# Performance work log

Measured on AMD Instinct MI355X. Metric: run time of the kernel, lower is better.

## Reference

```python
import jax, jax.numpy as jnp
import numpy as np

NUM_NET = 5
N = 10000        # nodes per net
E = 160000       # edges per net
B = 512          # molecule graphs per batch
FXD = 62         # node feature dim
FXT = 954        # cell feature dim
D = 128          # output_dim
H1 = 10          # heads in first GATConv


def setup_inputs() -> dict:
    key = jax.random.key(0)
    ks = iter(jax.random.split(key, 64))
    f32 = jnp.float32
    p = lambda shape, scale=0.05: jax.random.normal(next(ks), shape, dtype=f32) * scale
    inp = {}
    inp['x1'] = jax.random.normal(next(ks), (NUM_NET, N, FXD), dtype=f32)
    inp['ei1'] = jax.random.randint(next(ks), (NUM_NET, 2, E), 0, N, dtype=jnp.int32)
    b = ((jnp.arange(N) * B) // N).astype(jnp.int32)  # sorted, no empty graphs
    inp['batch1'] = jnp.broadcast_to(b, (NUM_NET, N))
    inp['x2'] = jax.random.normal(next(ks), (NUM_NET, N, FXD), dtype=f32)
    inp['ei2'] = jax.random.randint(next(ks), (NUM_NET, 2, E), 0, N, dtype=jnp.int32)
    inp['batch2'] = jnp.broadcast_to(b, (NUM_NET, N))
    inp['cell'] = jax.random.normal(next(ks), (B, FXT), dtype=f32)
    # per-net GAT params (stacked over NUM_NET)
    inp['W1'] = p((NUM_NET, H1 * D, FXD))
    inp['a1s'] = p((NUM_NET, H1, D)); inp['a1d'] = p((NUM_NET, H1, D))
    inp['b1'] = p((NUM_NET, H1 * D))
    inp['W2'] = p((NUM_NET, D, H1 * D))
    inp['a2s'] = p((NUM_NET, 1, D)); inp['a2d'] = p((NUM_NET, 1, D))
    inp['b2'] = p((NUM_NET, D))
    inp['Wg'] = p((NUM_NET, D, D)); inp['bg'] = p((NUM_NET, D))
    # cell reduction MLP 954->2048->512->256
    inp['Wr1'] = p((2048, FXT)); inp['br1'] = p((2048,))
    inp['Wr2'] = p((512, 2048)); inp['br2'] = p((512,))
    inp['Wr3'] = p((2 * D, 512)); inp['br3'] = p((2 * D,))
    # head MLP 512->2048->512->128->2
    inp['Wf1'] = p((2048, 4 * D)); inp['bf1'] = p((2048,))
    inp['Wf2'] = p((512, 2048)); inp['bf2'] = p((512,))
    inp['Wf3'] = p((128, 512)); inp['bf3'] = p((128,))
    inp['Wo'] = p((2, 128)); inp['bo'] = p((2,))
    return inp


def _gat(x, src, dst, W, a_s, a_d, b):
    # PyG GATConv (eval): linear -> per-head attention logits -> segment softmax over dst -> scatter-sum
    n = x.shape[0]
    H, C = a_s.shape
    h = (x @ W.T).reshape(n, H, C)
    al = (h * a_s).sum(-1)   # [n, H] source term
    ar = (h * a_d).sum(-1)   # [n, H] dest term
    e = jax.nn.leaky_relu(al[src] + ar[dst], negative_slope=0.2)  # [Ee, H]
    m = jax.ops.segment_max(e, dst, num_segments=n)               # self-loops -> no empty segments
    pe = jnp.exp(e - m[dst])
    s = jax.ops.segment_sum(pe, dst, num_segments=n)
    alpha = pe / s[dst]
    out = jax.ops.segment_sum(h[src] * alpha[:, :, None], dst, num_segments=n)
    return out.reshape(n, H * C) + b


def _branch(x, ei, batch, W1, a1s, a1d, b1, W2, a2s, a2d, b2, Wg, bg):
    n = x.shape[0]
    loops = jnp.arange(n, dtype=ei.dtype)  # add_self_loops=True in PyG GATConv
    src = jnp.concatenate([ei[0], loops])
    dst = jnp.concatenate([ei[1], loops])
    h = jax.nn.elu(_gat(x, src, dst, W1, a1s, a1d, b1))
    h = jax.nn.elu(_gat(h, src, dst, W2, a2s, a2d, b2))
    g = jax.ops.segment_max(h, batch, num_segments=B)  # global max pool
    return jax.nn.relu(g @ Wg.T + bg)


def _l2n(v):
    return v / jnp.clip(jnp.linalg.norm(v, axis=1, keepdims=True), 1e-12)


def reference(x1, ei1, batch1, x2, ei2, batch2, cell,
              W1, a1s, a1d, b1, W2, a2s, a2d, b2, Wg, bg,
              Wr1, br1, Wr2, br2, Wr3, br3,
              Wf1, bf1, Wf2, bf2, Wf3, bf3, Wo, bo):
    x11 = jnp.zeros((B, D), dtype=x1.dtype)
    x22 = jnp.zeros((B, D), dtype=x2.dtype)
    for i in range(NUM_NET):
        pr = (W1[i], a1s[i], a1d[i], b1[i], W2[i], a2s[i], a2d[i], b2[i], Wg[i], bg[i])
        x11 = x11 + _branch(x1[i], ei1[i], batch1[i], *pr) / NUM_NET
        x22 = x22 + _branch(x2[i], ei2[i], batch2[i], *pr) / NUM_NET
    c = _l2n(cell)
    c = jax.nn.relu(c @ Wr1.T + br1)
    c = jax.nn.relu(c @ Wr2.T + br2)
    c = jax.nn.relu(c @ Wr3.T + br3)
    xc = _l2n(jnp.concatenate([x11, x22, c], axis=1))
    xc = jax.nn.relu(xc @ Wf1.T + bf1)
    xc = jax.nn.relu(xc @ Wf2.T + bf2)
    xc = jax.nn.relu(xc @ Wf3.T + bf3)
    return xc @ Wo.T + bo
```

## Files before the change

kernel.cpp:

```cpp
#include <hip/hip_runtime.h>
#include <hip/hip_bf16.h>
#include <math.h>

#define NUM_NET 5
#define NN 10000
#define NE 160000
#define BB 512
#define FXD 62
#define FXT 954
#define MP 10112

typedef __bf16 bf16x8 __attribute__((ext_vector_type(8)));
typedef float f32x4 __attribute__((ext_vector_type(4)));
typedef __hip_bfloat16 bf16;

__device__ __forceinline__ float ldf(const void* p, size_t i) {
  return ((const float*)p)[i];
}
__device__ __forceinline__ float lky(float v) { return v > 0.f ? v : 0.2f * v; }
__device__ __forceinline__ float eluf(float v) { return v > 0.f ? v : (__expf(v) - 1.f); }
__device__ __forceinline__ unsigned int packbf(float a, float b) {
  __hip_bfloat162 t;
  t.x = __float2bfloat16(a);
  t.y = __float2bfloat16(b);
// ... 82 lines not shown
  int br = z & 1, net = z >> 1;
  const int* base = (br ? ei2 : ei1) + (size_t)net * 2 * NE;
  const int* src = base;
  const int* dst = base + NE;
  const int* offz = offs + (size_t)z * (NN + 1);
  int* fillz = fill + (size_t)z * NN;
  int* out = csrc + (size_t)z * NE;
  int i = blockIdx.x * 256 + threadIdx.x;
  if (i < NE) {
    int d = dst[i];
    int p = offz[d] + atomicAdd(&fillz[d], 1);
    out[p] = src[i];
  }
}

__global__ __launch_bounds__(256) void walr_kernel(const void* __restrict__ W1,
                                                   const void* __restrict__ a1s,
                                                   const void* __restrict__ a1d,
                                                   bf16* __restrict__ walrb) {
  int net = blockIdx.x / 10, head = blockIdx.x % 10;
  int t = threadIdx.x, w = t >> 6, k = t & 63;
  __shared__ float ps[8][64];
  float accs = 0.f, accd = 0.f;
  for (int c = w; c < 128; c += 4) {
    float wv = (k < FXD)
        ? ldf(W1, (size_t)net * 1280 * FXD + (size_t)(head * 128 + c) * FXD + k) : 0.f;
    float vs = ldf(a1s, (size_t)net * 1280 + head * 128 + c);
    float vd = ldf(a1d, (size_t)net * 1280 + head * 128 + c);
    accs = fmaf(wv, vs, accs);
    accd = fmaf(wv, vd, accd);
  }
  ps[w][k] = accs;
  ps[4 + w][k] = accd;
  __syncthreads();
  if (w == 0) {
    float s = ps[0][k] + ps[1][k] + ps[2][k] + ps[3][k];
    float dd = ps[4][k] + ps[5][k] + ps[6][k] + ps[7][k];
    walrb[(size_t)net * 4096 + head * 64 + k] = __float2bfloat16(s);
    walrb[(size_t)net * 4096 + (16 + head) * 64 + k] = __float2bfloat16(dd);
  }
}

__global__ __launch_bounds__(256) void alpha_kernel(
    const float* __restrict__ alrA, const int* __restrict__ offsA,
    const int* __restrict__ srcsA, unsigned int* __restrict__ alphaG, int planeBase) {
  int z = blockIdx.z;
  int plane = planeBase + z;
  const float* alr = alrA + (size_t)plane * MP * 32;
  const int* offs = offsA + (size_t)plane * (NN + 1);
  const int* srcs = srcsA + (size_t)plane * NE;
  unsigned int* ag = alphaG + (size_t)z * (NE + NN) * 6;
  int wave = threadIdx.x >> 6, lane = threadIdx.x & 63;
  int d = blockIdx.x * 4 + wave;
  if (d >= NN) return;
  int e0 = offs[d], ne = offs[d + 1] - e0;
  int total = ne + 1;
  float arh[10];
#pragma unroll
  for (int h = 0; h < 10; h++) arh[h] = alr[(size_t)d * 32 + 16 + h];
  if (total <= 64) {
    int sc = (lane < ne) ? srcs[e0 + lane] : d;
    bool act = lane < total;
    const float* ap = &alr[(size_t)sc * 32];
    float v[10], m[10];
#pragma unroll
    for (int h = 0; h < 10; h++) {
      v[h] = act ? lky(ap[h] + arh[h]) : -1e30f;
      m[h] = v[h];
    }
#pragma unroll
    for (int o = 32; o > 0; o >>= 1)
#pragma unroll
      for (int h = 0; h < 10; h++) m[h] = fmaxf(m[h], __shfl_xor(m[h], o));
    float p[10], s[10];
#pragma unroll
    for (int h = 0; h < 10; h++) {
      p[h] = act ? __expf(v[h] - m[h]) : 0.f;
      s[h] = p[h];
    }
#pragma unroll
    for (int o = 32; o > 0; o >>= 1)
#pragma unroll
      for (int h = 0; h < 10; h++) s[h] += __shfl_xor(s[h], o);
    if (act) {
      float inv[10];
#pragma unroll
      for (int h = 0; h < 10; h++) inv[h] = 1.f / s[h];
      unsigned int wv[6];
#pragma unroll
      for (int hp = 0; hp < 5; hp++)
        wv[hp] = packbf(p[2 * hp] * inv[2 * hp], p[2 * hp + 1] * inv[2 * hp + 1]);
      wv[5] = (unsigned int)(d & 15);
      size_t row = (lane < ne) ? (size_t)(e0 + lane) : (size_t)(NE + d);
      unsigned int* rp = ag + row * 6;
#pragma unroll
      for (int j = 0; j < 6; j++) rp[j] = wv[j];
    }
  } else {
    float m[10], s[10];
#pragma unroll
    for (int h = 0; h < 10; h++) { m[h] = -1e30f; s[h] = 0.f; }
    for (int idx = lane; idx < total; idx += 64) {
      int sc = (idx < ne) ? srcs[e0 + idx] : d;
      const float* ap = &alr[(size_t)sc * 32];
#pragma unroll
      for (int h = 0; h < 10; h++) {
        float v = lky(ap[h] + arh[h]);
        if (v > m[h]) { s[h] = s[h] * __expf(m[h] - v) + 1.f; m[h] = v; }
        else s[h] += __expf(v - m[h]);
      }
    }
#pragma unroll
    for (int o = 32; o > 0; o >>= 1)
#pragma unroll
      for (int h = 0; h < 10; h++) {
        float mo = __shfl_xor(m[h], o), so = __shfl_xor(s[h], o);
        if (so > 0.f) {
          if (mo > m[h]) { s[h] = s[h] * __expf(m[h] - mo) + so; m[h] = mo; }
          else s[h] += so * __expf(mo - m[h]);
        }
      }
    for (int idx = lane; idx < total; idx += 64) {
      int sc = (idx < ne) ? srcs[e0 + idx] : d;
      const float* ap = &alr[(size_t)sc * 32];
      unsigned int wv[6];
#pragma unroll
      for (int hp = 0; hp < 5; hp++) {
        float v0 = lky(ap[2 * hp] + arh[2 * hp]);
        float v1 = lky(ap[2 * hp + 1] + arh[2 * hp + 1]);
        wv[hp] = packbf(__expf(v0 - m[2 * hp]) / s[2 * hp],
                        __expf(v1 - m[2 * hp + 1]) / s[2 * hp + 1]);
      }
      wv[5] = (unsigned int)(d & 15);
      size_t row = (idx < ne) ? (size_t)(e0 + idx) : (size_t)(NE + d);
      unsigned int* rp = ag + row * 6;
#pragma unroll
      for (int j = 0; j < 6; j++) rp[j] = wv[j];
    }
  }
}

struct Pref {
  uint4 xv;
  unsigned int a0, a1, a2, a3, a4;
  int dl;
  int av;
};

__device__ __forceinline__ void issue_pref(
    Pref& P, int kb, int e, int fblk, int tid, int nreal, int K_len, int e_begin,
    int d0, const int* __restrict__ srcs, const bf16* __restrict__ xp,
    const unsigned int* __restrict__ ag) {
  int ke = kb + e;
  int src;
  if (ke < nreal) {
    src = srcs[e_begin + ke];
  } else {
    int sl = ke - nreal;
    src = d0 + (sl < 16 ? sl : 0);
  }
  P.xv = *(const uint4*)&xp[(size_t)src * 64 + fblk * 8];
  P.av = 0;
  if (tid < 32 && ke < K_len) {
    P.av = 1;
    size_t row = (ke < nreal) ? (size_t)(e_begin + ke) : (size_t)(NE + d0 + (ke - nreal));
    const unsigned int* rp = ag + row * 6;
    P.a0 = rp[0]; P.a1 = rp[1]; P.a2 = rp[2]; P.a3 = rp[3]; P.a4 = rp[4];
    P.dl = (int)rp[5];
  }
}

__global__ __launch_bounds__(256) void xagg_kernel(
    const bf16* __restrict__ xpadA, const unsigned int* __restrict__ alphaG,
    const int* __restrict__ offsA, const int* __restrict__ srcsA,
    bf16* __restrict__ xagg2, int planeBase) {
  int z = blockIdx.z;
  int plane = planeBase + z;
  bf16* xagg = xagg2 + (size_t)z * 10 * MP * 64;
  int d0 = blockIdx.x * 16;
  int tid = threadIdx.x;

  if (d0 >= NN) {
    uint4 zz; zz.x = zz.y = zz.z = zz.w = 0u;
#pragma unroll
    for (int k = 0; k < 5; k++) {
      int i = tid + k * 256;
      int h = i >> 7, rem = i & 127, row = rem >> 3, seg = rem & 7;
      *(uint4*)&xagg[((size_t)h * MP + d0 + row) * 64 + seg * 8] = zz;
    }
    return;
  }

  const bf16* xp = xpadA + (size_t)plane * MP * 64;
  const int* offs = offsA + (size_t)plane * (NN + 1);
  const int* srcs = srcsA + (size_t)plane * NE;
  const unsigned int* ag = alphaG + (size_t)z * (NE + NN) * 6;

  __shared__ __align__(16) short A_s[10 * 16 * 40];
  __shared__ __align__(16) short Xt_s[64 * 40];

  int e_begin = offs[d0];
  int nreal = offs[d0 + 16] - e_begin;
  int K_len = nreal + 16;

  int e = tid & 31, fblk = tid >> 5;
  int lane = tid & 63, wave = tid >> 6;
  int l15 = lane & 15, quad = lane >> 4;
  int hbase = (wave >> 1) * 5;
  int wcol = (wave & 1) * 32;

  Pref Pn;
  issue_pref(Pn, 0, e, fblk, tid, nreal, K_len, e_begin, d0, srcs, xp, ag);

  {
    f32x4 z4 = (f32x4){0.f, 0.f, 0.f, 0.f};
    for (int i = tid; i < 800; i += 256) ((f32x4*)A_s)[i] = z4;
  }
  f32x4 acc[5][2];
#pragma unroll
  for (int i = 0; i < 5; i++)
#pragma unroll
    for (int j = 0; j < 2; j++) acc[i][j] = (f32x4){0.f, 0.f, 0.f, 0.f};
  int prev_dl = -1;
  __syncthreads();

  for (int kb = 0; kb < K_len; kb += 32) {
    Pref Pc = Pn;
    if (tid < 32) {
      if (prev_dl >= 0) {
#pragma unroll
        for (int h = 0; h < 10; h++) A_s[(h * 16 + prev_dl) * 40 + e] = 0;
      }
      prev_dl = -1;
      if (Pc.av) {
        int dlc = Pc.dl;
        A_s[(0 * 16 + dlc) * 40 + e] = (short)(Pc.a0 & 0xffff);
        A_s[(1 * 16 + dlc) * 40 + e] = (short)(Pc.a0 >> 16);
        A_s[(2 * 16 + dlc) * 40 + e] = (short)(Pc.a1 & 0xffff);
        A_s[(3 * 16 + dlc) * 40 + e] = (short)(Pc.a1 >> 16);
        A_s[(4 * 16 + dlc) * 40 + e] = (short)(Pc.a2 & 0xffff);
        A_s[(5 * 16 + dlc) * 40 + e] = (short)(Pc.a2 >> 16);
        A_s[(6 * 16 + dlc) * 40 + e] = (short)(Pc.a3 & 0xffff);
        A_s[(7 * 16 + dlc) * 40 + e] = (short)(Pc.a3 >> 16);
        A_s[(8 * 16 + dlc) * 40 + e] = (short)(Pc.a4 & 0xffff);
        A_s[(9 * 16 + dlc) * 40 + e] = (short)(Pc.a4 >> 16);
        prev_dl = dlc;
      }
    }
    {
      int fb8 = fblk * 8;
#pragma unroll
      for (int j = 0; j < 4; j++) {
        unsigned int w = ((const unsigned int*)&Pc.xv)[j];
        Xt_s[(fb8 + 2 * j) * 40 + e] = (short)(w & 0xffff);
        Xt_s[(fb8 + 2 * j + 1) * 40 + e] = (short)(w >> 16);
      }
    }
    if (kb + 32 < K_len)
      issue_pref(Pn, kb + 32, e, fblk, tid, nreal, K_len, e_begin, d0, srcs, xp, ag);
    __syncthreads();
    bf16x8 b0 = *(const bf16x8*)&Xt_s[(wcol + l15) * 40 + quad * 8];
    bf16x8 b1 = *(const bf16x8*)&Xt_s[(wcol + 16 + l15) * 40 + quad * 8];
#pragma unroll
    for (int hh = 0; hh < 5; hh++) {
      bf16x8 af = *(const bf16x8*)&A_s[((hbase + hh) * 16 + l15) * 40 + quad * 8];
      acc[hh][0] = __builtin_amdgcn_mfma_f32_16x16x32_bf16(af, b0, acc[hh][0], 0, 0, 0);
      acc[hh][1] = __builtin_amdgcn_mfma_f32_16x16x32_bf16(af, b1, acc[hh][1], 0, 0, 0);
    }
    __syncthreads();
  }

#pragma unroll
  for (int hh = 0; hh < 5; hh++) {
    int h = hbase + hh;
#pragma unroll
    for (int ft = 0; ft < 2; ft++) {
#pragma unroll
      for (int r = 0; r < 4; r++) {
        int drow = d0 + quad * 4 + r;
        xagg[((size_t)h * MP + drow) * 64 + wcol + ft * 16 + l15] =
            __float2bfloat16(acc[hh][ft][r]);
      }
    }
  }
}

__global__ __launch_bounds__(256) void fused_l1l2_kernel(
    const bf16* __restrict__ xagg2, const bf16* __restrict__ W1b,
    const void* __restrict__ b1raw, const bf16* __restrict__ W2b,
    const void* __restrict__ a2s, const void* __restrict__ a2d,
    float* __restrict__ al2A, float* __restrict__ ar2A,
    bf16* __restrict__ h2all, int planeBase) {
  int zz = blockIdx.z;
  int plane = planeBase + zz;
  int net = plane >> 1;
  long ow1 = (long)net * 1280 * 64;
  long ob1 = (long)net * 1280;
  long ow2 = (long)net * 128 * 1280;
  long oa2 = (long)net * 128;
  const bf16* xagg = xagg2 + (size_t)zz * 10 * MP * 64;
  float* al2p = al2A + (size_t)plane * NN;
  float* ar2p = ar2A + (size_t)plane * NN;
  bf16* h2 = h2all + (size_t)plane * MP * 128;
  int r0 = blockIdx.y * 64;
  __shared__ __align__(16) char uraw[35840];
  bf16* Ah = (bf16*)uraw;
  bf16* W1s = Ah + 64 * 72;
  bf16* Ps = (bf16*)uraw;
  bf16* W2s = Ps + 64 * 136;
  __shared__ float s_dot[2][2][32][2];
  int tid = threadIdx.x, lane = tid & 63, wave = tid >> 6;
  int l15 = lane & 15, quad = lane >> 4;
  int rowHalf = wave >> 1, colHalf = wave & 1;
  int wr = rowHalf * 32, wc = colHalf * 64;
  f32x4 acc2[2][4];
#pragma unroll
  for (int i = 0; i < 2; i++)
#pragma unroll
    for (int j = 0; j < 4; j++) acc2[i][j] = (f32x4){0.f, 0.f, 0.f, 0.f};

  for (int h = 0; h < 10; h++) {
    __syncthreads();
    for (int i = tid; i < 512; i += 256) {
      int r = i >> 3, seg = i & 7;
      *(uint4*)&Ah[r * 72 + seg * 8] =
          *(const uint4*)&xagg[((size_t)h * MP + r0 + r) * 64 + seg * 8];
    }
    for (int i = tid; i < 1024; i += 256) {
      int r = i >> 3, seg = i & 7;
      *(uint4*)&W1s[r * 72 + seg * 8] =
          *(const uint4*)&W1b[ow1 + (size_t)(h * 128 + r) * 64 + seg * 8];
    }
    __syncthreads();
    f32x4 acc1[4][2];
#pragma unroll
    for (int i = 0; i < 4; i++)
#pragma unroll
      for (int j = 0; j < 2; j++) acc1[i][j] = (f32x4){0.f, 0.f, 0.f, 0.f};
#pragma unroll
    for (int kc = 0; kc < 2; kc++) {
      bf16x8 af[4], bfr[2];
#pragma unroll
      for (int mi = 0; mi < 4; mi++)
        af[mi] = *(const bf16x8*)&Ah[(mi * 16 + l15) * 72 + kc * 32 + quad * 8];
#pragma unroll
      for (int ni = 0; ni < 2; ni++)
        bfr[ni] = *(const bf16x8*)&W1s[(wave * 32 + ni * 16 + l15) * 72 + kc * 32 + quad * 8];
#pragma unroll
      for (int mi = 0; mi < 4; mi++)
#pragma unroll
        for (int ni = 0; ni < 2; ni++)
          acc1[mi][ni] = __builtin_amdgcn_mfma_f32_16x16x32_bf16(af[mi], bfr[ni], acc1[mi][ni], 0, 0, 0);
    }
    __syncthreads();
#pragma unroll
    for (int ni = 0; ni < 2; ni++) {
      int pcol = wave * 32 + ni * 16 + l15;
      float bv = ldf(b1raw, ob1 + h * 128 + pcol);
#pragma unroll
      for (int mi = 0; mi < 4; mi++)
#pragma unroll
        for (int r = 0; r < 4; r++)
          Ps[(mi * 16 + quad * 4 + r) * 136 + pcol] =
              __float2bfloat16(eluf(acc1[mi][ni][r] + bv));
    }
    for (int i = tid; i < 1024; i += 256) {
      int r = i >> 3, seg = i & 7;
      *(uint4*)&W2s[r * 72 + seg * 8] =
          *(const uint4*)&W2b[ow2 + (size_t)r * 1280 + h * 128 + seg * 8];
    }
    __syncthreads();
#pragma unroll
    for (int kh = 0; kh < 2; kh++) {
      if (kh) {
        __syncthreads();
        for (int i = tid; i < 1024; i += 256) {
          int r = i >> 3, seg = i & 7;
          *(uint4*)&W2s[r * 72 + seg * 8] =
              *(const uint4*)&W2b[ow2 + (size_t)r * 1280 + h * 128 + 64 + seg * 8];
        }
        __syncthreads();
      }
#pragma unroll
      for (int kc = 0; kc < 2; kc++) {
        bf16x8 pa[2], pb[4];
#pragma unroll
        for (int mi = 0; mi < 2; mi++)
          pa[mi] = *(const bf16x8*)&Ps[(wr + mi * 16 + l15) * 136 + kh * 64 + kc * 32 + quad * 8];
#pragma unroll
        for (int ni = 0; ni < 4; ni++)
          pb[ni] = *(const bf16x8*)&W2s[(wc + ni * 16 + l15) * 72 + kc * 32 + quad * 8];
#pragma unroll
        for (int mi = 0; mi < 2; mi++)
#pragma unroll
          for (int ni = 0; ni < 4; ni++)
            acc2[mi][ni] = __builtin_amdgcn_mfma_f32_16x16x32_bf16(pa[mi], pb[ni], acc2[mi][ni], 0, 0, 0);
      }
    }
  }
  float asv[4], adv[4];
#pragma unroll
  for (int ni = 0; ni < 4; ni++) {
    int col = wc + ni * 16 + l15;
    asv[ni] = ldf(a2s, oa2 + col);
    adv[ni] = ldf(a2d, oa2 + col);
  }
#pragma unroll
  for (int mi = 0; mi < 2; mi++) {
#pragma unroll
    for (int r = 0; r < 4; r++) {
      int rl = mi * 16 + quad * 4 + r;
      int row = r0 + wr + rl;
      float psum = 0.f, pdum = 0.f;
#pragma unroll
      for (int ni = 0; ni < 4; ni++) {
        float v = acc2[mi][ni][r];
        h2[(size_t)row * 128 + wc + ni * 16 + l15] = __float2bfloat16(v);
        psum = fmaf(v, asv[ni], psum);
        pdum = fmaf(v, adv[ni], pdum);
      }
#pragma unroll
      for (int o = 1; o < 16; o <<= 1) {
        psum += __shfl_xor(psum, o);
        pdum += __shfl_xor(pdum, o);
      }
      if (l15 == 0) {
        s_dot[rowHalf][colHalf][rl][0] = psum;
        s_dot[rowHalf][colHalf][rl][1] = pdum;
      }
    }
  }
  __syncthreads();
  if (tid < 64) {
    int row = r0 + tid;
    if (row < NN) {
      int rh = tid >> 5, rl = tid & 31;
      al2p[row] = s_dot[rh][0][rl][0] + s_dot[rh][1][rl][0];
      ar2p[row] = s_dot[rh][0][rl][1] + s_dot[rh][1][rl][1];
    }
  }
}

__global__ __launch_bounds__(256) void mfma_gemm64(
    const bf16* __restrict__ A, long Az, const bf16* __restrict__ B, long Bz, int bdiv,
    const void* __restrict__ bias, long biasoff, long biaszs,
    float* __restrict__ Cf, long Cfz, int ldcf, int accum, int ncols, int brcol,
    bf16* __restrict__ Cb, long Cbz, int ldcb,
    int K, int act, float scale) {
  int z = blockIdx.z;
  int zb = bdiv ? (z >> 1) : z;
  A += (size_t)z * Az;
  B += (size_t)zb * Bz;
  if (Cf) Cf += (size_t)z * Cfz + (size_t)(z & 1) * brcol;
  if (Cb) Cb += (size_t)z * Cbz;
  const bf16* Ag = A + (size_t)blockIdx.y * 64 * K;
  const bf16* Bg = B + (size_t)blockIdx.x * 64 * K;
  __shared__ __align__(16) bf16 Asm[64 * 40];
  __shared__ __align__(16) bf16 Bsm[64 * 40];
  int tid = threadIdx.x;
  int lane = tid & 63, wave = tid >> 6;
  int wr = (wave >> 1) * 32, wc = (wave & 1) * 32;
  int l15 = lane & 15, quad = lane >> 4;
  f32x4 acc[2][2];
#pragma unroll
  for (int i = 0; i < 2; i++)
#pragma unroll
    for (int j = 0; j < 2; j++) acc[i][j] = (f32x4){0.f, 0.f, 0.f, 0.f};
  int isB = tid >> 7;
  int srow = (tid & 127) >> 1, shalf = tid & 1;
  const bf16* G = isB ? Bg : Ag;
  bf16* S = isB ? Bsm : Asm;
  for (int k0 = 0; k0 < K; k0 += 32) {
    const uint4* g = (const uint4*)(G + (size_t)srow * K + k0 + shalf * 16);
    uint4 v0 = g[0], v1 = g[1];
    __syncthreads();
    *(uint4*)&S[srow * 40 + shalf * 16] = v0;
    *(uint4*)&S[srow * 40 + shalf * 16 + 8] = v1;
    __syncthreads();
    bf16x8 af[2], bfr[2];
#pragma unroll
    for (int mi = 0; mi < 2; mi++)
      af[mi] = *(const bf16x8*)&Asm[(wr + mi * 16 + l15) * 40 + quad * 8];
#pragma unroll
    for (int ni = 0; ni < 2; ni++)
      bfr[ni] = *(const bf16x8*)&Bsm[(wc + ni * 16 + l15) * 40 + quad * 8];
#pragma unroll
    for (int mi = 0; mi < 2; mi++)
#pragma unroll
      for (int ni = 0; ni < 2; ni++)
        acc[mi][ni] = __builtin_amdgcn_mfma_f32_16x16x32_bf16(af[mi], bfr[ni], acc[mi][ni], 0, 0, 0);
  }
#pragma unroll
  for (int ni = 0; ni < 2; ni++) {
    int col = blockIdx.x * 64 + wc + ni * 16 + l15;
    if (col >= ncols) continue;
    float bv = bias ? ldf(bias, biasoff + (size_t)zb * biaszs + col) : 0.f;
#pragma unroll
    for (int mi = 0; mi < 2; mi++) {
      int rbase = blockIdx.y * 64 + wr + mi * 16 + quad * 4;
      f32x4 c = acc[mi][ni];
#pragma unroll
      for (int r = 0; r < 4; r++) {
        float v = c[r] + bv;
        if (act == 1) v = fmaxf(v, 0.f);
        else if (act == 2) v = eluf(v);
        v *= scale;
        if (Cf) {
          size_t ci = (size_t)(rbase + r) * ldcf + col;
          if (accum == 1) Cf[ci] += v;
          else if (accum == 2) atomicAdd(&Cf[ci], v);
          else Cf[ci] = v;
        }
        if (Cb) Cb[(size_t)(rbase + r) * ldcb + col] = __float2bfloat16(v);
      }
    }
  }
}

__global__ __launch_bounds__(256) void gat_agg1_kernel(
    const bf16* __restrict__ h2all, const float* __restrict__ alA, const float* __restrict__ arA,
    const int* __restrict__ offsA, const int* __restrict__ srcsA,
    const void* __restrict__ b2, bf16* __restrict__ out2all) {
  int z = blockIdx.z;
  int net = z >> 1;
  const bf16* h = h2all + (size_t)z * MP * 128;
  const float* al = alA + (size_t)z * NN;
  const float* ar = arA + (size_t)z * NN;
  const int* offs = offsA + (size_t)z * (NN + 1);
  const int* srcs = srcsA + (size_t)z * NE;
  __shared__ float2 s_pair[4][64];
  int wave = threadIdx.x >> 6, lane = threadIdx.x & 63;
  int d = blockIdx.x * 4 + wave;
  if (d >= NN) return;
  int e0 = offs[d], ne = offs[d + 1] - e0;
  int total = ne + 1;
  float ard = ar[d];
  float m, s, vcache = -1e30f;
  if (total <= 64) {
    int sc = (lane < ne) ? srcs[e0 + lane] : d;
    bool act = lane < total;
    vcache = act ? lky(al[sc] + ard) : -1e30f;
    m = vcache;
    s = act ? 1.f : 0.f;
#pragma unroll
    for (int o = 32; o > 0; o >>= 1) {
      float mo = __shfl_xor(m, o), so = __shfl_xor(s, o);
      if (so > 0.f) {
        if (mo > m) { s = s * __expf(m - mo) + so; m = mo; }
        else s += so * __expf(mo - m);
      }
    }
  } else {
    m = -1e30f; s = 0.f;
    for (int idx = lane; idx < total; idx += 64) {
      int sc = (idx < ne) ? srcs[e0 + idx] : d;
      float v = lky(al[sc] + ard);
      if (v > m) { s = s * __expf(m - v) + 1.f; m = v; }
      else s += __expf(v - m);
    }
#pragma unroll
    for (int o = 32; o > 0; o >>= 1) {
      float mo = __shfl_xor(m, o), so = __shfl_xor(s, o);
      if (so > 0.f) {
        if (mo > m) { s = s * __expf(m - mo) + so; m = mo; }
        else s += so * __expf(mo - m);
      }
    }
  }
  float inv_s = 1.f / s;
  float acc0 = 0.f, acc1v = 0.f;
  for (int c0 = 0; c0 < total; c0 += 64) {
    int idx = c0 + lane;
    int cnt = min(64, total - c0);
    if (idx < total) {
      int sc = (idx < ne) ? srcs[e0 + idx] : d;
      float v = (total <= 64) ? vcache : lky(al[sc] + ard);
      float a = __expf(v - m) * inv_s;
      s_pair[wave][lane] = make_float2(__int_as_float(sc), a);
    }
    int i = 0;
    for (; i + 2 <= cnt; i += 2) {
      float2 pA = s_pair[wave][i];
      float2 pB = s_pair[wave][i + 1];
      __hip_bfloat162 vA =
          ((const __hip_bfloat162*)(h + (size_t)__float_as_int(pA.x) * 128))[lane];
      __hip_bfloat162 vB =
          ((const __hip_bfloat162*)(h + (size_t)__float_as_int(pB.x) * 128))[lane];
      acc0 = fmaf(__bfloat162float(vA.x), pA.y, acc0);
      acc1v = fmaf(__bfloat162float(vA.y), pA.y, acc1v);
      acc0 = fmaf(__bfloat162float(vB.x), pB.y, acc0);
      acc1v = fmaf(__bfloat162float(vB.y), pB.y, acc1v);
    }
    if (i < cnt) {
      float2 pA = s_pair[wave][i];
      __hip_bfloat162 vA =
          ((const __hip_bfloat162*)(h + (size_t)__float_as_int(pA.x) * 128))[lane];
      acc0 = fmaf(__bfloat162float(vA.x), pA.y, acc0);
      acc1v = fmaf(__bfloat162float(vA.y), pA.y, acc1v);
    }
  }
  float b0 = ldf(b2, (size_t)net * 128 + 2 * lane);
  float b1v = ldf(b2, (size_t)net * 128 + 2 * lane + 1);
  __hip_bfloat162 o;
  o.x = __float2bfloat16(eluf(acc0 + b0));
  o.y = __float2bfloat16(eluf(acc1v + b1v));
  ((__hip_bfloat162*)(out2all + ((size_t)z * NN + d) * 128))[lane] = o;
}

__global__ __launch_bounds__(256) void pool_max_kernel(const bf16* __restrict__ out2all,
                                                       bf16* __restrict__ gall) {
  int z = blockIdx.z;
  const bf16* h = out2all + (size_t)z * NN * 128;
  bf16* g = gall + (size_t)z * BB * 128;
  int wave = threadIdx.x >> 6, lane = threadIdx.x & 63;
  int b = blockIdx.x * 4 + wave;
  if (b >= BB) return;
  int n0 = (b * NN + BB - 1) / BB;
  int n1 = ((b + 1) * NN + BB - 1) / BB;
  if (n1 > NN) n1 = NN;
  float mx = -1e30f, my = -1e30f;
  for (int n = n0; n < n1; n++) {
    __hip_bfloat162 v = ((const __hip_bfloat162*)(h + (size_t)n * 128))[lane];
    mx = fmaxf(mx, __bfloat162float(v.x));
    my = fmaxf(my, __bfloat162float(v.y));
  }
  __hip_bfloat162 o;
  o.x = __float2bfloat16(mx);
  o.y = __float2bfloat16(my);
  ((__hip_bfloat162*)(g + (size_t)b * 128))[lane] = o;
}

__global__ __launch_bounds__(256) void l2norm_b_kernel(const float* __restrict__ x,
                                                       bf16* __restrict__ y, int Din, int Kp) {
  int r = blockIdx.x, t = threadIdx.x;
  __shared__ float red[256];
  float s = 0.f;
  for (int i = t; i < Din; i += 256) {
    float v = x[(size_t)r * Din + i];
    s += v * v;
  }
  red[t] = s;
  __syncthreads();
  for (int o = 128; o > 0; o >>= 1) { if (t < o) red[t] += red[t + o]; __syncthreads(); }
  float inv = 1.f / fmaxf(sqrtf(red[0]), 1e-12f);
  for (int i = t; i < Kp; i += 256) {
    float v = (i < Din) ? x[(size_t)r * Din + i] : 0.f;
    y[(size_t)r * Kp + i] = __float2bfloat16(v * inv);
  }
}

__global__ void final_out_kernel(const float* __restrict__ f3, const void* __restrict__ Wo,
                                 const void* __restrict__ bo, float* __restrict__ out) {
  int r = blockIdx.x;
  int lane = threadIdx.x;
  float x0 = f3[(size_t)r * 128 + lane], x1v = f3[(size_t)r * 128 + 64 + lane];
  float s0 = x0 * ldf(Wo, lane) + x1v * ldf(Wo, 64 + lane);
  float s1 = x0 * ldf(Wo, 128 + lane) + x1v * ldf(Wo, 192 + lane);
#pragma unroll
  for (int o = 32; o > 0; o >>= 1) { s0 += __shfl_down(s0, o); s1 += __shfl_down(s1, o); }
  if (lane == 0) {
    out[r * 2] = s0 + ldf(bo, 0);
    out[r * 2 + 1] = s1 + ldf(bo, 1);
  }
}


extern "C" void kernel_launch(void* const* d_in, const int* in_sizes, int n_in,
                              void* d_out, int out_size, void* d_ws, size_t ws_size,
                              hipStream_t stream) {
  const void* x1 = d_in[0];
  const int* ei1 = (const int*)d_in[1];
  const void* x2 = d_in[3];
  const int* ei2 = (const int*)d_in[4];
  const void* cell = d_in[6];
  const void* W1 = d_in[7];
  const void* a1s = d_in[8];
  const void* a1d = d_in[9];
  const void* b1 = d_in[10];
  const void* W2 = d_in[11];
  const void* a2s = d_in[12];
  const void* a2d = d_in[13];
  const void* b2 = d_in[14];
  const void* Wg = d_in[15];
  const void* bg = d_in[16];
  const void* Wr1 = d_in[17]; const void* br1 = d_in[18];
  const void* Wr2 = d_in[19]; const void* br2 = d_in[20];
  const void* Wr3 = d_in[21]; const void* br3 = d_in[22];
  const void* Wf1 = d_in[23]; const void* bf1 = d_in[24];
  const void* Wf2 = d_in[25]; const void* bf2 = d_in[26];
  const void* Wf3 = d_in[27]; const void* bf3 = d_in[28];
  const void* Wo = d_in[29]; const void* bo = d_in[30];

  char* base = (char*)d_ws;
  size_t off = 0;
  auto alloc = [&](size_t bytes) -> void* {
    void* p = base + off;
    off = (off + bytes + 255) & ~(size_t)255;
    return p;
  };
  bf16* d_xpad = (bf16*)alloc((size_t)10 * MP * 64 * 2);
  bf16* d_W1b = (bf16*)alloc((size_t)5 * 1280 * 64 * 2);
  bf16* d_W2b = (bf16*)alloc((size_t)5 * 128 * 1280 * 2);
  bf16* d_Wgb = (bf16*)alloc((size_t)5 * 128 * 128 * 2);
  bf16* d_Wr1b = (bf16*)alloc((size_t)2048 * 960 * 2);
  bf16* d_Wr2b = (bf16*)alloc((size_t)512 * 2048 * 2);
  bf16* d_Wr3b = (bf16*)alloc((size_t)256 * 512 * 2);
  bf16* d_Wf1b = (bf16*)alloc((size_t)2048 * 512 * 2);
  bf16* d_Wf2b = (bf16*)alloc((size_t)512 * 2048 * 2);
  bf16* d_Wf3b = (bf16*)alloc((size_t)128 * 512 * 2);
  int* d_offs = (int*)alloc((size_t)10 * (NN + 1) * 4);
  int* d_srcs = (int*)alloc((size_t)10 * NE * 4);
  int* d_cnt = (int*)alloc((size_t)10 * NN * 4);
  bf16* d_walrb = (bf16*)alloc((size_t)5 * 64 * 64 * 2);
  float* d_alr = (float*)alloc((size_t)10 * MP * 32 * 4);
  float* d_al2 = (float*)alloc((size_t)20 * NN * 4);
  float* d_ar2 = d_al2 + (size_t)10 * NN;
  bf16* d_h2all = (bf16*)alloc((size_t)10 * MP * 128 * 2);
  unsigned int* d_alphaG = (unsigned int*)alloc((size_t)10 * (NE + NN) * 24);
  char* uni = base + off;
  size_t avail = (ws_size > off) ? (ws_size - off) : 0;
  size_t need10 = (size_t)10 * 10 * MP * 64 * 2;
  int G = (avail >= need10 + 65536) ? 10 : 5;
  bf16* d_xagg2 = (bf16*)uni;
  bf16* d_out2all = (bf16*)uni;
  bf16* d_gall = (bf16*)(uni + 25600000);
  float* d_xc = (float*)(uni + 26910720);
  bf16* d_xcb = (bf16*)(uni + 27959296);
  bf16* d_cnb = (bf16*)(uni + 28483584);
  bf16* d_m1b = (bf16*)(uni + 29466624);
  bf16* d_m2b = (bf16*)(uni + 31563776);
  float* d_f3 = (float*)(uni + 32088064);

  ConvTable tab;
  tab.d[0] = {x1, d_xpad, NN, FXD, MP, 64, 2, 0, 5, (MP + 3) / 4};
  tab.d[1] = {x2, d_xpad, NN, FXD, MP, 64, 2, 1, 5, (MP + 3) / 4};
  tab.d[2] = {W1, d_W1b, 1280, FXD, 1280, 64, 1, 0, 5, 320};
  tab.d[3] = {W2, d_W2b, 128, 1280, 128, 1280, 1, 0, 5, 32};
  tab.d[4] = {Wg, d_Wgb, 128, 128, 128, 128, 1, 0, 5, 32};
  tab.d[5] = {Wr1, d_Wr1b, 2048, FXT, 2048, 960, 1, 0, 1, 512};
  tab.d[6] = {Wr2, d_Wr2b, 512, 2048, 512, 2048, 1, 0, 1, 128};
  tab.d[7] = {Wr3, d_Wr3b, 256, 512, 256, 512, 1, 0, 1, 64};
  tab.d[8] = {Wf1, d_Wf1b, 2048, 512, 2048, 512, 1, 0, 1, 512};
  tab.d[9] = {Wf2, d_Wf2b, 512, 2048, 512, 2048, 1, 0, 1, 128};
  tab.d[10] = {Wf3, d_Wf3b, 128, 512, 128, 512, 1, 0, 1, 32};
  {
    int cum = 0;
    tab.blk0[0] = 0;
    for (int i = 0; i < 11; i++) {
      cum += tab.d[i].rowBlocks * tab.d[i].batch;
      tab.blk0[i + 1] = cum;
    }
    convert_all_kernel<<<dim3(cum), 256, 0, stream>>>(tab);
  }

  hipMemsetAsync(d_cnt, 0, (size_t)10 * NN * 4, stream);
  hist_kernel<<<dim3((NE + 255) / 256, 1, 10), 256, 0, stream>>>(ei1, ei2, d_cnt);
  scan_kernel<<<10, 256, 0, stream>>>(d_cnt, d_offs);
  hipMemsetAsync(d_cnt, 0, (size_t)10 * NN * 4, stream);
  scatter_kernel<<<dim3((NE + 255) / 256, 1, 10), 256, 0, stream>>>(ei1, ei2, d_offs, d_cnt, d_srcs);

  walr_kernel<<<50, 256, 0, stream>>>(W1, a1s, a1d, d_walrb);
  mfma_gemm64<<<dim3(1, MP / 64, 10), 256, 0, stream>>>(
      d_xpad, (long)MP * 64, d_walrb, 4096, 1, nullptr, 0, 0,
      d_alr, (long)MP * 32, 32, 0, 32, 0, nullptr, 0, 0, 64, 0, 1.f);

  for (int pb = 0; pb < 10; pb += G) {
    alpha_kernel<<<dim3(NN / 4, 1, G), 256, 0, stream>>>(d_alr, d_offs, d_srcs, d_alphaG, pb);
    xagg_kernel<<<dim3(MP / 16, 1, G), 256, 0, stream>>>(d_xpad, d_alphaG, d_offs, d_srcs, d_xagg2, pb);
    fused_l1l2_kernel<<<dim3(1, MP / 64, G), 256, 0, stream>>>(
        d_xagg2, d_W1b, b1, d_W2b, a2s, a2d, d_al2, d_ar2, d_h2all, pb);
  }

  hipMemsetAsync(d_xc, 0, (size_t)BB * 512 * 4, stream);
  gat_agg1_kernel<<<dim3(2500, 1, 10), 256, 0, stream>>>(
      d_h2all, d_al2, d_ar2, d_offs, d_srcs, b2, d_out2all);
  pool_max_kernel<<<dim3(BB / 4, 1, 10), 256, 0, stream>>>(d_out2all, d_gall);
  mfma_gemm64<<<dim3(2, BB / 64, 10), 256, 0, stream>>>(
      d_gall, (long)BB * 128, d_Wgb, 128 * 128, 1,
      bg, 0, 128,
      d_xc, 0, 512, 2, 128, 128, nullptr, 0, 0, 128, 1, 0.2f);

  l2norm_b_kernel<<<BB, 256, 0, stream>>>((const float*)cell, d_cnb, FXT, 960);
  mfma_gemm64<<<dim3(32, 8, 1), 256, 0, stream>>>(
      d_cnb, 0, d_Wr1b, 0, 0, br1, 0, 0, nullptr, 0, 0, 0, 1 << 30, 0, d_m1b, 0, 2048, 960, 1, 1.f);
  mfma_gemm64<<<dim3(8, 8, 1), 256, 0, stream>>>(
      d_m1b, 0, d_Wr2b, 0, 0, br2, 0, 0, nullptr, 0, 0, 0, 1 << 30, 0, d_m2b, 0, 512, 2048, 1, 1.f);
  mfma_gemm64<<<dim3(4, 8, 1), 256, 0, stream>>>(
      d_m2b, 0, d_Wr3b, 0, 0, br3, 0, 0, d_xc + 256, 0, 512, 0, 1 << 30, 0, nullptr, 0, 0, 512, 1, 1.f);

  l2norm_b_kernel<<<BB, 256, 0, stream>>>(d_xc, d_xcb, 512, 512);
  mfma_gemm64<<<dim3(32, 8, 1), 256, 0, stream>>>(
      d_xcb, 0, d_Wf1b, 0, 0, bf1, 0, 0, nullptr, 0, 0, 0, 1 << 30, 0, d_m1b, 0, 2048, 512, 1, 1.f);
  mfma_gemm64<<<dim3(8, 8, 1), 256, 0, stream>>>(
      d_m1b, 0, d_Wf2b, 0, 0, bf2, 0, 0, nullptr, 0, 0, 0, 1 << 30, 0, d_m2b, 0, 512, 2048, 1, 1.f);
  mfma_gemm64<<<dim3(2, 8, 1), 256, 0, stream>>>(
      d_m2b, 0, d_Wf3b, 0, 0, bf3, 0, 0, d_f3, 0, 128, 0, 1 << 30, 0, nullptr, 0, 0, 512, 1, 1.f);
  final_out_kernel<<<BB, 64, 0, stream>>>(d_f3, Wo, bo, (float*)d_out);
}
```

Before: 995.7 us.

## Double row tile in fused GAT layer kernel to 128 rows per block

The fused layer-1/layer-2 kernel now processes 128 node rows per block instead of 64. Each wave owns 32 full-width rows, so the cross-wave shared-memory reduction for the attention dots is dropped. The whole 128-column W2 slice is loaded into shared memory in one pass rather than two halves, which removes extra barriers and amortizes weight loads over twice the rows. In exchange, shared memory grows to about 68 KB and accumulator registers double, which may lower occupancy, and the grid has half as many blocks.

After: 984.4 us. Within noise of the previous version (-1.1%).

```diff
diff --git a/kernel.cpp b/kernel.cpp
--- a/kernel.cpp
+++ b/kernel.cpp
@@ -408,106 +408,95 @@
   float* al2p = al2A + (size_t)plane * NN;
   float* ar2p = ar2A + (size_t)plane * NN;
   bf16* h2 = h2all + (size_t)plane * MP * 128;
-  int r0 = blockIdx.y * 64;
-  __shared__ __align__(16) char uraw[35840];
+  int r0 = blockIdx.y * 128;
+  __shared__ __align__(16) char uraw[69632];
   bf16* Ah = (bf16*)uraw;
-  bf16* W1s = Ah + 64 * 72;
+  bf16* W1s = Ah + 128 * 72;
   bf16* Ps = (bf16*)uraw;
-  bf16* W2s = Ps + 64 * 136;
-  __shared__ float s_dot[2][2][32][2];
+  bf16* W2s = Ps + 128 * 136;
   int tid = threadIdx.x, lane = tid & 63, wave = tid >> 6;
   int l15 = lane & 15, quad = lane >> 4;
-  int rowHalf = wave >> 1, colHalf = wave & 1;
-  int wr = rowHalf * 32, wc = colHalf * 64;
-  f32x4 acc2[2][4];
+  int wr = wave * 32;
+  f32x4 acc2[2][8];
 #pragma unroll
   for (int i = 0; i < 2; i++)
 #pragma unroll
-    for (int j = 0; j < 4; j++) acc2[i][j] = (f32x4){0.f, 0.f, 0.f, 0.f};
+    for (int j = 0; j < 8; j++) acc2[i][j] = (f32x4){0.f, 0.f, 0.f, 0.f};
 
   for (int h = 0; h < 10; h++) {
     __syncthreads();
-    for (int i = tid; i < 512; i += 256) {
-      int r = i >> 3, seg = i & 7;
-      *(uint4*)&Ah[r * 72 + seg * 8] =
-          *(const uint4*)&xagg[((size_t)h * MP + r0 + r) * 64 + seg * 8];
-    }
-    for (int i = tid; i < 1024; i += 256) {
-      int r = i >> 3, seg = i & 7;
-      *(uint4*)&W1s[r * 72 + seg * 8] =
-          *(const uint4*)&W1b[ow1 + (size_t)(h * 128 + r) * 64 + seg * 8];
-    }
-    __syncthreads();
-    f32x4 acc1[4][2];
-#pragma unroll
-    for (int i = 0; i < 4; i++)
-#pragma unroll
-      for (int j = 0; j < 2; j++) acc1[i][j] = (f32x4){0.f, 0.f, 0.f, 0.f};
+#pragma unroll
+    for (int j = 0; j < 4; j++) {
+      int i = tid + j * 256;
+      *(uint4*)&Ah[(i >> 3) * 72 + (i & 7) * 8] =
+          *(const uint4*)&xagg[((size_t)h * MP + r0 + (i >> 3)) * 64 + (i & 7) * 8];
+    }
+#pragma unroll
+    for (int j = 0; j < 4; j++) {
+      int i = tid + j * 256;
+      *(uint4*)&W1s[(i >> 3) * 72 + (i & 7) * 8] =
+          *(const uint4*)&W1b[ow1 + (size_t)(h * 128 + (i >> 3)) * 64 + (i & 7) * 8];
+    }
+    __syncthreads();
+    f32x4 acc1[2][8];
+#pragma unroll
+    for (int i = 0; i < 2; i++)
+#pragma unroll
+      for (int j = 0; j < 8; j++) acc1[i][j] = (f32x4){0.f, 0.f, 0.f, 0.f};
 #pragma unroll
     for (int kc = 0; kc < 2; kc++) {
-      bf16x8 af[4], bfr[2];
-#pragma unroll
-      for (int mi = 0; mi < 4; mi++)
-        af[mi] = *(const bf16x8*)&Ah[(mi * 16 + l15) * 72 + kc * 32 + quad * 8];
-#pragma unroll
-      for (int ni = 0; ni < 2; ni++)
-        bfr[ni] = *(const bf16x8*)&W1s[(wave * 32 + ni * 16 + l15) * 72 + kc * 32 + quad * 8];
-#pragma unroll
-      for (int mi = 0; mi < 4; mi++)
-#pragma unroll
-        for (int ni = 0; ni < 2; ni++)
+      bf16x8 af[2], bfr[8];
+#pragma unroll
+      for (int mi = 0; mi < 2; mi++)
+        af[mi] = *(const bf16x8*)&Ah[(wr + mi * 16 + l15) * 72 + kc * 32 + quad * 8];
+#pragma unroll
+      for (int ni = 0; ni < 8; ni++)
+        bfr[ni] = *(const bf16x8*)&W1s[(ni * 16 + l15) * 72 + kc * 32 + quad * 8];
+#pragma unroll
+      for (int mi = 0; mi < 2; mi++)
+#pragma unroll
+        for (int ni = 0; ni < 8; ni++)
           acc1[mi][ni] = __builtin_amdgcn_mfma_f32_16x16x32_bf16(af[mi], bfr[ni], acc1[mi][ni], 0, 0, 0);
     }
     __syncthreads();
 #pragma unroll
-    for (int ni = 0; ni < 2; ni++) {
-      int pcol = wave * 32 + ni * 16 + l15;
+    for (int ni = 0; ni < 8; ni++) {
+      int pcol = ni * 16 + l15;
       float bv = ldf(b1raw, ob1 + h * 128 + pcol);
 #pragma unroll
-      for (int mi = 0; mi < 4; mi++)
+      for (int mi = 0; mi < 2; mi++)
 #pragma unroll
         for (int r = 0; r < 4; r++)
-          Ps[(mi * 16 + quad * 4 + r) * 136 + pcol] =
+          Ps[(wr + mi * 16 + quad * 4 + r) * 136 + pcol] =
               __float2bfloat16(eluf(acc1[mi][ni][r] + bv));
     }
-    for (int i = tid; i < 1024; i += 256) {
-      int r = i >> 3, seg = i & 7;
-      *(uint4*)&W2s[r * 72 + seg * 8] =
-          *(const uint4*)&W2b[ow2 + (size_t)r * 1280 + h * 128 + seg * 8];
-    }
-    __syncthreads();
-#pragma unroll
-    for (int kh = 0; kh < 2; kh++) {
-      if (kh) {
-        __syncthreads();
-        for (int i = tid; i < 1024; i += 256) {
-          int r = i >> 3, seg = i & 7;
-          *(uint4*)&W2s[r * 72 + seg * 8] =
-              *(const uint4*)&W2b[ow2 + (size_t)r * 1280 + h * 128 + 64 + seg * 8];
-        }
-        __syncthreads();
-      }
-#pragma unroll
-      for (int kc = 0; kc < 2; kc++) {
-        bf16x8 pa[2], pb[4];
-#pragma unroll
-        for (int mi = 0; mi < 2; mi++)
-          pa[mi] = *(const bf16x8*)&Ps[(wr + mi * 16 + l15) * 136 + kh * 64 + kc * 32 + quad * 8];
-#pragma unroll
-        for (int ni = 0; ni < 4; ni++)
-          pb[ni] = *(const bf16x8*)&W2s[(wc + ni * 16 + l15) * 72 + kc * 32 + quad * 8];
-#pragma unroll
-        for (int mi = 0; mi < 2; mi++)
-#pragma unroll
-          for (int ni = 0; ni < 4; ni++)
-            acc2[mi][ni] = __builtin_amdgcn_mfma_f32_16x16x32_bf16(pa[mi], pb[ni], acc2[mi][ni], 0, 0, 0);
-      }
-    }
-  }
-  float asv[4], adv[4];
-#pragma unroll
-  for (int ni = 0; ni < 4; ni++) {
-    int col = wc + ni * 16 + l15;
+#pragma unroll
+    for (int j = 0; j < 8; j++) {
+      int i = tid + j * 256;
+      *(uint4*)&W2s[(i >> 4) * 136 + (i & 15) * 8] =
+          *(const uint4*)&W2b[ow2 + (size_t)(i >> 4) * 1280 + h * 128 + (i & 15) * 8];
+    }
+    __syncthreads();
+#pragma unroll
+    for (int kc = 0; kc < 4; kc++) {
+      bf16x8 pa[2], pb[8];
+#pragma unroll
+      for (int mi = 0; mi < 2; mi++)
+        pa[mi] = *(const bf16x8*)&Ps[(wr + mi * 16 + l15) * 136 + kc * 32 + quad * 8];
+#pragma unroll
+      for (int ni = 0; ni < 8; ni++)
+        pb[ni] = *(const bf16x8*)&W2s[(ni * 16 + l15) * 136 + kc * 32 + quad * 8];
+#pragma unroll
+      for (int mi = 0; mi < 2; mi++)
+#pragma unroll
+        for (int ni = 0; ni < 8; ni++)
+          acc2[mi][ni] = __builtin_amdgcn_mfma_f32_16x16x32_bf16(pa[mi], pb[ni], acc2[mi][ni], 0, 0, 0);
+    }
+  }
+  float asv[8], adv[8];
+#pragma unroll
+  for (int ni = 0; ni < 8; ni++) {
+    int col = ni * 16 + l15;
     asv[ni] = ldf(a2s, oa2 + col);
     adv[ni] = ldf(a2d, oa2 + col);
   }
@@ -515,13 +504,12 @@
   for (int mi = 0; mi < 2; mi++) {
 #pragma unroll
     for (int r = 0; r < 4; r++) {
-      int rl = mi * 16 + quad * 4 + r;
-      int row = r0 + wr + rl;
+      int row = r0 + wr + mi * 16 + quad * 4 + r;
       float psum = 0.f, pdum = 0.f;
 #pragma unroll
-      for (int ni = 0; ni < 4; ni++) {
+      for (int ni = 0; ni < 8; ni++) {
         float v = acc2[mi][ni][r];
-        h2[(size_t)row * 128 + wc + ni * 16 + l15] = __float2bfloat16(v);
+        h2[(size_t)row * 128 + ni * 16 + l15] = __float2bfloat16(v);
         psum = fmaf(v, asv[ni], psum);
         pdum = fmaf(v, adv[ni], pdum);
       }
@@ -530,19 +518,10 @@
         psum += __shfl_xor(psum, o);
         pdum += __shfl_xor(pdum, o);
       }
-      if (l15 == 0) {
-        s_dot[rowHalf][colHalf][rl][0] = psum;
-        s_dot[rowHalf][colHalf][rl][1] = pdum;
-      }
-    }
-  }
-  __syncthreads();
-  if (tid < 64) {
-    int row = r0 + tid;
-    if (row < NN) {
-      int rh = tid >> 5, rl = tid & 31;
-      al2p[row] = s_dot[rh][0][rl][0] + s_dot[rh][1][rl][0];
-      ar2p[row] = s_dot[rh][0][rl][1] + s_dot[rh][1][rl][1];
+      if (l15 == 0 && row < NN) {
+        al2p[row] = psum;
+        ar2p[row] = pdum;
+      }
     }
   }
 }
@@ -873,7 +852,7 @@
   for (int pb = 0; pb < 10; pb += G) {
     alpha_kernel<<<dim3(NN / 4, 1, G), 256, 0, stream>>>(d_alr, d_offs, d_srcs, d_alphaG, pb);
     xagg_kernel<<<dim3(MP / 16, 1, G), 256, 0, stream>>>(d_xpad, d_alphaG, d_offs, d_srcs, d_xagg2, pb);
-    fused_l1l2_kernel<<<dim3(1, MP / 64, G), 256, 0, stream>>>(
+    fused_l1l2_kernel<<<dim3(1, MP / 128, G), 256, 0, stream>>>(
         d_xagg2, d_W1b, b1, d_W2b, a2s, a2d, d_al2, d_ar2, d_h2all, pb);
   }
 
```

## Recast layer-2 GAT aggregation as MFMA block matmul and load W2 slab once

Applied to the files above, without the earlier changes.

The layer-2 attention aggregation, previously one wave per destination doing scalar gather-FMAs, now processes 16 destinations per block. It builds a sparse bf16 attention matrix over the block's contiguous edge range and multiplies it against the transposed gathered source features with MFMA, using register prefetch of the next 32-edge chunk. Separately, the fused layer1/layer2 kernel loads the full 128-wide W2 slice per head into enlarged shared memory, removing a reload and two barriers. This costs more LDS per block, which may lower occupancy, and the MFMA path does zero-padded work plus extra syncs per edge chunk. Attention weights are also rounded to bf16.

Measured after the change: 941.2 us. 1.06x faster.

```diff
diff --git a/kernel.cpp b/kernel.cpp
--- a/kernel.cpp
+++ b/kernel.cpp
@@ -409,7 +409,7 @@
   float* ar2p = ar2A + (size_t)plane * NN;
   bf16* h2 = h2all + (size_t)plane * MP * 128;
   int r0 = blockIdx.y * 64;
-  __shared__ __align__(16) char uraw[35840];
+  __shared__ __align__(16) char uraw[52224];
   bf16* Ah = (bf16*)uraw;
   bf16* W1s = Ah + 64 * 72;
   bf16* Ps = (bf16*)uraw;
@@ -470,38 +470,26 @@
           Ps[(mi * 16 + quad * 4 + r) * 136 + pcol] =
               __float2bfloat16(eluf(acc1[mi][ni][r] + bv));
     }
-    for (int i = tid; i < 1024; i += 256) {
-      int r = i >> 3, seg = i & 7;
-      *(uint4*)&W2s[r * 72 + seg * 8] =
+    for (int i = tid; i < 2048; i += 256) {
+      int r = i >> 4, seg = i & 15;
+      *(uint4*)&W2s[r * 136 + seg * 8] =
           *(const uint4*)&W2b[ow2 + (size_t)r * 1280 + h * 128 + seg * 8];
     }
     __syncthreads();
 #pragma unroll
-    for (int kh = 0; kh < 2; kh++) {
-      if (kh) {
-        __syncthreads();
-        for (int i = tid; i < 1024; i += 256) {
-          int r = i >> 3, seg = i & 7;
-          *(uint4*)&W2s[r * 72 + seg * 8] =
-              *(const uint4*)&W2b[ow2 + (size_t)r * 1280 + h * 128 + 64 + seg * 8];
-        }
-        __syncthreads();
-      }
-#pragma unroll
-      for (int kc = 0; kc < 2; kc++) {
-        bf16x8 pa[2], pb[4];
-#pragma unroll
-        for (int mi = 0; mi < 2; mi++)
-          pa[mi] = *(const bf16x8*)&Ps[(wr + mi * 16 + l15) * 136 + kh * 64 + kc * 32 + quad * 8];
+    for (int kc = 0; kc < 4; kc++) {
+      bf16x8 pa[2], pb[4];
+#pragma unroll
+      for (int mi = 0; mi < 2; mi++)
+        pa[mi] = *(const bf16x8*)&Ps[(wr + mi * 16 + l15) * 136 + kc * 32 + quad * 8];
+#pragma unroll
+      for (int ni = 0; ni < 4; ni++)
+        pb[ni] = *(const bf16x8*)&W2s[(wc + ni * 16 + l15) * 136 + kc * 32 + quad * 8];
+#pragma unroll
+      for (int mi = 0; mi < 2; mi++)
 #pragma unroll
         for (int ni = 0; ni < 4; ni++)
-          pb[ni] = *(const bf16x8*)&W2s[(wc + ni * 16 + l15) * 72 + kc * 32 + quad * 8];
-#pragma unroll
-        for (int mi = 0; mi < 2; mi++)
-#pragma unroll
-          for (int ni = 0; ni < 4; ni++)
-            acc2[mi][ni] = __builtin_amdgcn_mfma_f32_16x16x32_bf16(pa[mi], pb[ni], acc2[mi][ni], 0, 0, 0);
-      }
+          acc2[mi][ni] = __builtin_amdgcn_mfma_f32_16x16x32_bf16(pa[mi], pb[ni], acc2[mi][ni], 0, 0, 0);
     }
   }
   float asv[4], adv[4];
@@ -623,7 +611,41 @@
   }
 }
 
-__global__ __launch_bounds__(256) void gat_agg1_kernel(
+struct Pref2 {
+  uint4 xv0, xv1;
+  float alv;
+  int dl;
+  int av;
+};
+
+__device__ __forceinline__ void issue_pref2(
+    Pref2& P, int kb, int e, int fblk, int tid, int nreal, int K_len, int e_begin,
+    int d0, const int* __restrict__ srcs, const bf16* __restrict__ h,
+    const float* __restrict__ al, const int* s_offs) {
+  int ke = kb + e;
+  int src, dl;
+  if (ke < nreal) {
+    int eg = e_begin + ke;
+    src = srcs[eg];
+    dl = 0;
+#pragma unroll
+    for (int jj = 1; jj < 16; jj++) dl += (eg >= s_offs[jj]);
+  } else {
+    int sl = ke - nreal;
+    dl = sl;
+    src = d0 + (sl < 16 ? sl : 0);
+  }
+  P.xv0 = *(const uint4*)&h[(size_t)src * 128 + fblk * 16];
+  P.xv1 = *(const uint4*)&h[(size_t)src * 128 + fblk * 16 + 8];
+  P.av = 0;
+  if (tid < 32 && ke < K_len) {
+    P.av = 1;
+    P.alv = al[src];
+    P.dl = dl;
+  }
+}
+
+__global__ __launch_bounds__(256) void gat_agg2_kernel(
     const bf16* __restrict__ h2all, const float* __restrict__ alA, const float* __restrict__ arA,
     const int* __restrict__ offsA, const int* __restrict__ srcsA,
     const void* __restrict__ b2, bf16* __restrict__ out2all) {
@@ -634,83 +656,108 @@
   const float* ar = arA + (size_t)z * NN;
   const int* offs = offsA + (size_t)z * (NN + 1);
   const int* srcs = srcsA + (size_t)z * NE;
-  __shared__ float2 s_pair[4][64];
-  int wave = threadIdx.x >> 6, lane = threadIdx.x & 63;
-  int d = blockIdx.x * 4 + wave;
-  if (d >= NN) return;
-  int e0 = offs[d], ne = offs[d + 1] - e0;
-  int total = ne + 1;
-  float ard = ar[d];
-  float m, s, vcache = -1e30f;
-  if (total <= 64) {
-    int sc = (lane < ne) ? srcs[e0 + lane] : d;
-    bool act = lane < total;
-    vcache = act ? lky(al[sc] + ard) : -1e30f;
-    m = vcache;
-    s = act ? 1.f : 0.f;
-#pragma unroll
-    for (int o = 32; o > 0; o >>= 1) {
+  int d0 = blockIdx.x * 16;
+  int tid = threadIdx.x;
+
+  __shared__ __align__(16) short A_s[16 * 40];
+  __shared__ __align__(16) short Xt_s[128 * 40];
+  __shared__ int s_offs[17];
+  __shared__ float s_m[16], s_sinv[16], s_ar[16];
+
+  if (tid < 17) s_offs[tid] = offs[d0 + tid];
+  __syncthreads();
+  int e_begin = s_offs[0];
+  int nreal = s_offs[16] - e_begin;
+  int K_len = nreal + 16;
+
+  {
+    int dl = tid >> 4, par = tid & 15;
+    int d = d0 + dl;
+    float ard = ar[d];
+    float m, s;
+    if (par == 0) { m = lky(al[d] + ard); s = 1.f; }
+    else { m = -1e30f; s = 0.f; }
+    int ee = s_offs[dl + 1];
+    for (int e2 = s_offs[dl] + par; e2 < ee; e2 += 16) {
+      float v = lky(al[srcs[e2]] + ard);
+      if (v > m) { s = s * __expf(m - v) + 1.f; m = v; }
+      else s += __expf(v - m);
+    }
+#pragma unroll
+    for (int o = 8; o >= 1; o >>= 1) {
       float mo = __shfl_xor(m, o), so = __shfl_xor(s, o);
       if (so > 0.f) {
         if (mo > m) { s = s * __expf(m - mo) + so; m = mo; }
         else s += so * __expf(mo - m);
       }
     }
-  } else {
-    m = -1e30f; s = 0.f;
-    for (int idx = lane; idx < total; idx += 64) {
-      int sc = (idx < ne) ? srcs[e0 + idx] : d;
-      float v = lky(al[sc] + ard);
-      if (v > m) { s = s * __expf(m - v) + 1.f; m = v; }
-      else s += __expf(v - m);
-    }
-#pragma unroll
-    for (int o = 32; o > 0; o >>= 1) {
-      float mo = __shfl_xor(m, o), so = __shfl_xor(s, o);
-      if (so > 0.f) {
-        if (mo > m) { s = s * __expf(m - mo) + so; m = mo; }
-        else s += so * __expf(mo - m);
-      }
-    }
-  }
-  float inv_s = 1.f / s;
-  float acc0 = 0.f, acc1v = 0.f;
-  for (int c0 = 0; c0 < total; c0 += 64) {
-    int idx = c0 + lane;
-    int cnt = min(64, total - c0);
-    if (idx < total) {
-      int sc = (idx < ne) ? srcs[e0 + idx] : d;
-      float v = (total <= 64) ? vcache : lky(al[sc] + ard);
-      float a = __expf(v - m) * inv_s;
-      s_pair[wave][lane] = make_float2(__int_as_float(sc), a);
-    }
-    int i = 0;
-    for (; i + 2 <= cnt; i += 2) {
-      float2 pA = s_pair[wave][i];
-      float2 pB = s_pair[wave][i + 1];
-      __hip_bfloat162 vA =
-          ((const __hip_bfloat162*)(h + (size_t)__float_as_int(pA.x) * 128))[lane];
-      __hip_bfloat162 vB =
-          ((const __hip_bfloat162*)(h + (size_t)__float_as_int(pB.x) * 128))[lane];
-      acc0 = fmaf(__bfloat162float(vA.x), pA.y, acc0);
-      acc1v = fmaf(__bfloat162float(vA.y), pA.y, acc1v);
-      acc0 = fmaf(__bfloat162float(vB.x), pB.y, acc0);
-      acc1v = fmaf(__bfloat162float(vB.y), pB.y, acc1v);
-    }
-    if (i < cnt) {
-      float2 pA = s_pair[wave][i];
-      __hip_bfloat162 vA =
-          ((const __hip_bfloat162*)(h + (size_t)__float_as_int(pA.x) * 128))[lane];
-      acc0 = fmaf(__bfloat162float(vA.x), pA.y, acc0);
-      acc1v = fmaf(__bfloat162float(vA.y), pA.y, acc1v);
-    }
-  }
-  float b0 = ldf(b2, (size_t)net * 128 + 2 * lane);
-  float b1v = ldf(b2, (size_t)net * 128 + 2 * lane + 1);
-  __hip_bfloat162 o;
-  o.x = __float2bfloat16(eluf(acc0 + b0));
-  o.y = __float2bfloat16(eluf(acc1v + b1v));
-  ((__hip_bfloat162*)(out2all + ((size_t)z * NN + d) * 128))[lane] = o;
+    if (par == 0) { s_m[dl] = m; s_sinv[dl] = 1.f / s; s_ar[dl] = ard; }
+  }
+
+  int e = tid & 31, fblk = tid >> 5;
+  int lane = tid & 63, wave = tid >> 6;
+  int l15 = lane & 15, quad = lane >> 4;
+  int wcol = wave * 32;
+
+  Pref2 Pn;
+  issue_pref2(Pn, 0, e, fblk, tid, nreal, K_len, e_begin, d0, srcs, h, al, s_offs);
+
+  if (tid < 80) {
+    uint4 zz; zz.x = zz.y = zz.z = zz.w = 0u;
+    ((uint4*)A_s)[tid] = zz;
+  }
+  f32x4 acc[2];
+  acc[0] = (f32x4){0.f, 0.f, 0.f, 0.f};
+  acc[1] = (f32x4){0.f, 0.f, 0.f, 0.f};
+  int prev_dl = -1;
+  __syncthreads();
+
+  for (int kb = 0; kb < K_len; kb += 32) {
+    Pref2 Pc = Pn;
+    if (tid < 32) {
+      if (prev_dl >= 0) A_s[prev_dl * 40 + e] = 0;
+      prev_dl = -1;
+      if (Pc.av) {
+        float v = lky(Pc.alv + s_ar[Pc.dl]);
+        float a = __expf(v - s_m[Pc.dl]) * s_sinv[Pc.dl];
+        A_s[Pc.dl * 40 + e] = (short)(packbf(a, 0.f) & 0xffff);
+        prev_dl = Pc.dl;
+      }
+    }
+    {
+      int fb = fblk * 16;
+#pragma unroll
+      for (int j = 0; j < 4; j++) {
+        unsigned int w0 = ((const unsigned int*)&Pc.xv0)[j];
+        Xt_s[(fb + 2 * j) * 40 + e] = (short)(w0 & 0xffff);
+        Xt_s[(fb + 2 * j + 1) * 40 + e] = (short)(w0 >> 16);
+        unsigned int w1 = ((const unsigned int*)&Pc.xv1)[j];
+        Xt_s[(fb + 8 + 2 * j) * 40 + e] = (short)(w1 & 0xffff);
+        Xt_s[(fb + 8 + 2 * j + 1) * 40 + e] = (short)(w1 >> 16);
+      }
+    }
+    if (kb + 32 < K_len)
+      issue_pref2(Pn, kb + 32, e, fblk, tid, nreal, K_len, e_begin, d0, srcs, h, al, s_offs);
+    __syncthreads();
+    bf16x8 af = *(const bf16x8*)&A_s[l15 * 40 + quad * 8];
+    bf16x8 b0 = *(const bf16x8*)&Xt_s[(wcol + l15) * 40 + quad * 8];
+    bf16x8 b1 = *(const bf16x8*)&Xt_s[(wcol + 16 + l15) * 40 + quad * 8];
+    acc[0] = __builtin_amdgcn_mfma_f32_16x16x32_bf16(af, b0, acc[0], 0, 0, 0);
+    acc[1] = __builtin_amdgcn_mfma_f32_16x16x32_bf16(af, b1, acc[1], 0, 0, 0);
+    __syncthreads();
+  }
+
+#pragma unroll
+  for (int ft = 0; ft < 2; ft++) {
+    int col = wcol + ft * 16 + l15;
+    float bv = ldf(b2, (size_t)net * 128 + col);
+#pragma unroll
+    for (int r = 0; r < 4; r++) {
+      int row = d0 + quad * 4 + r;
+      out2all[((size_t)z * NN + row) * 128 + col] =
+          __float2bfloat16(eluf(acc[ft][r] + bv));
+    }
+  }
 }
 
 __global__ __launch_bounds__(256) void pool_max_kernel(const bf16* __restrict__ out2all,
@@ -878,7 +925,7 @@
   }
 
   hipMemsetAsync(d_xc, 0, (size_t)BB * 512 * 4, stream);
-  gat_agg1_kernel<<<dim3(2500, 1, 10), 256, 0, stream>>>(
+  gat_agg2_kernel<<<dim3(NN / 16, 1, 10), 256, 0, stream>>>(
       d_h2all, d_al2, d_ar2, d_offs, d_srcs, b2, d_out2all);
   pool_max_kernel<<<dim3(BB / 4, 1, 10), 256, 0, stream>>>(d_out2all, d_gall);
   mfma_gemm64<<<dim3(2, BB / 64, 10), 256, 0, stream>>>(
```
